# Performance work log

Measured on AMD Instinct MI355X. Metric: run time of the kernel, lower is better.

## Reference

```python
import math
import jax, jax.numpy as jnp
import numpy as np

B, T = 65536, 34
VOCAB, TOK_DIM, POS_DIM, D_MODEL, FFN_DIM, HEAD_DIM = 14, 2, 3, 5, 2, 5
EPS = 1e-5

def _pos_flat_idx():
    # replicate _build_pos_map: 10 digits, Z_HI, 10 digits, Z_HI, 10 digits, special0, special1
    sources, indices = [], []
    for _ in range(3):
        for i in range(10):
            sources.append(0); indices.append(i)
        sources.append(2); indices.append(len([s for s in sources if s == 2]) - 1)
    # fix: the torch code appends (2,0),(2,1) after first two digit blocks and (1,0),(2,2) after the third
    sources, indices = [], []
    for i in range(10): sources.append(0); indices.append(i)
    sources.append(2); indices.append(0)
    for i in range(10): sources.append(0); indices.append(i)
    sources.append(2); indices.append(1)
    for i in range(10): sources.append(0); indices.append(i)
    sources.append(1); indices.append(0)
    sources.append(2); indices.append(2)
    src = np.array(sources); idx = np.array(indices)
    # table layout: rows 0..9 digit_pos, row 10 z_hi_pos, rows 11..13 special (learned0, learned1, eos)
    offs = np.array([0, 10, 11])
    return offs[src] + idx  # (34,)

POS_FLAT = jnp.asarray(_pos_flat_idx())
CAUSAL = jnp.tril(jnp.ones((T, T), dtype=bool))

def _rms(x, w):
    return x * jax.lax.rsqrt(jnp.mean(x * x, -1, keepdims=True) + EPS) * w

def setup_inputs():
    key = jax.random.key(0)
    ks = jax.random.split(key, 16)
    n = lambda i, shape: jax.random.normal(ks[i], shape, jnp.float32) * 0.5
    return {
        'idx': jax.random.randint(ks[0], (B, T), 0, VOCAB),
        'tok_emb': n(1, (VOCAB, TOK_DIM)),
        'spiral_amp': jnp.float32(1.0),
        'spiral_phase': jnp.float32(0.1),
        'spiral_slope': jnp.float32(1.0 / 9.0),
        'spiral_offset': jnp.float32(0.05),
        'pos_corr_slope': jnp.float32(0.01),
        'pos_corr_intercept': jnp.float32(0.02),
        'z_hi_pos': n(2, (1, POS_DIM)),
        'special_pos': n(3, (2, POS_DIM)),
        'q_w': n(4, (HEAD_DIM, POS_DIM)),
        'v_w': n(5, (HEAD_DIM, TOK_DIM)),
        'out_A': n(6, (HEAD_DIM, 2)),
        'out_B': n(7, (2, D_MODEL)),
        'q_phase': n(8, (1,)),
        'ln1_w': jnp.ones((D_MODEL,), jnp.float32),
        'ln2_w': jnp.ones((D_MODEL,), jnp.float32),
        'lnf_w': jnp.ones((D_MODEL,), jnp.float32),
        'fc1_w': n(9, (FFN_DIM, D_MODEL)),
        'fc1_b': n(10, (FFN_DIM,)),
        'fc2_w': n(11, (D_MODEL, FFN_DIM)),
        'fc2_b': n(12, (D_MODEL,)),
        'head_w': n(13, (TOK_DIM, D_MODEL)),
    }

def reference(idx, tok_emb, spiral_amp, spiral_phase, spiral_slope, spiral_offset,
              pos_corr_slope, pos_corr_intercept, z_hi_pos, special_pos,
              q_w, v_w, out_A, out_B, q_phase, ln1_w, ln2_w, lnf_w,
              fc1_w, fc1_b, fc2_w, fc2_b, head_w):
    # learned spiral digit positions (10, 3)
    i = jnp.arange(10, dtype=jnp.float32)
    angle = 2.0 * math.pi * i / 10.0 + spiral_phase
    base = jnp.stack([spiral_amp * jnp.cos(angle),
                      spiral_amp * jnp.sin(angle),
                      spiral_slope * i + spiral_offset], -1)
    corr = pos_corr_intercept + pos_corr_slope * i
    digit_pos = base * (1.0 + corr)[:, None]
    table = jnp.concatenate([digit_pos, z_hi_pos, special_pos,
                             jnp.zeros((1, POS_DIM), jnp.float32)], 0)  # (14, 3)
    pos = table[POS_FLAT]  # (T, 3)

    tok = tok_emb[idx]  # (B, T, 2)
    x = jnp.concatenate([tok, jnp.broadcast_to(pos, (idx.shape[0], T, POS_DIM))], -1)  # (B,T,5)

    h = _rms(x, ln1_w)
    q = jnp.einsum('btp,dp->btd', h[..., TOK_DIM:], q_w)  # (B,T,5)
    k = q  # q_proj applied to same input for both q and k
    v = jnp.einsum('btp,dp->btd', h[..., :TOK_DIM], v_w)  # (B,T,5)

    # per-head 2D rotation on first 4 dims (HEAD_DIM//2 = 2 pairs), dim 4 unchanged
    c, s = jnp.cos(q_phase[0]), jnp.sin(q_phase[0])
    q0, q1 = q[..., 0:4:2], q[..., 1:4:2]
    q_rot = jnp.concatenate([
        jnp.stack([q0 * c - q1 * s, q0 * s + q1 * c], -1).reshape(q.shape[:-1] + (4,)),
        q[..., 4:]], -1)

    att = jnp.einsum('btd,bsd->bts', q_rot, k) / math.sqrt(HEAD_DIM)
    att = jnp.where(CAUSAL, att, -jnp.inf)
    att = jax.nn.softmax(att, -1)
    out = jnp.einsum('bts,bsd->btd', att, v)  # (B,T,5)

    x = x + (out @ out_A) @ out_B  # low-rank out_proj
    hh = _rms(x, ln2_w)
    x = x + (jax.nn.gelu(hh @ fc1_w.T + fc1_b, approximate=False) @ fc2_w.T + fc2_b)
    x = _rms(x, lnf_w)
    return (x @ head_w.T) @ tok_emb.T  # (B, T, 14)
```

## Files before the change

kernel.cpp:

```cpp
#include <hip/hip_runtime.h>
#include <math.h>

#define T_SEQ 34
#define NTOK 14
#define NE (T_SEQ * NTOK)

__global__ __launch_bounds__(256) void micro_fused_kernel(
    const int* __restrict__ idx,
    const float* __restrict__ tok_emb,
    const float* __restrict__ s_amp, const float* __restrict__ s_phase,
    const float* __restrict__ s_slope, const float* __restrict__ s_offset,
    const float* __restrict__ pc_slope, const float* __restrict__ pc_int,
    const float* __restrict__ z_hi, const float* __restrict__ spec,
    const float* __restrict__ q_w, const float* __restrict__ v_w,
    const float* __restrict__ out_A, const float* __restrict__ out_B,
    const float* __restrict__ q_phase,
    const float* __restrict__ ln1_w, const float* __restrict__ ln2_w,
    const float* __restrict__ lnf_w,
    const float* __restrict__ fc1_w, const float* __restrict__ fc1_b,
    const float* __restrict__ fc2_w, const float* __restrict__ fc2_b,
    const float* __restrict__ head_w,
    float* __restrict__ out, int N)
{
    __shared__ float H8[NE * 8];
    __shared__ float C3[NE * 4];
    __shared__ float PosT[T_SEQ * 3];
    __shared__ float TE[NTOK * 2];
    __shared__ float PMs[10];
    __shared__ float Ws[5 * NTOK];
    __shared__ float ln2s[5], lnfs[5], fc1ws[10], fc1bs[2], fc2ws[10], fc2bs[5];
    __shared__ int toks[9 * T_SEQ];

    const int tid = threadIdx.x;

    {
        const float amp = s_amp[0], ph = s_phase[0], slp = s_slope[0], off = s_offset[0];
        const float pcs = pc_slope[0], pci = pc_int[0];
        const float cph = cosf(q_phase[0]), sph = sinf(q_phase[0]);
        const float invs5 = 0.44721359549995793f;
        for (int e = tid; e < NE; e += 256) {
            int t = e / NTOK, tk = e - t * NTOK;
            float px, py, pz;
            if (t == 33)      { px = 0.f;     py = 0.f;     pz = 0.f; }
            else if (t == 32) { px = z_hi[0]; py = z_hi[1]; pz = z_hi[2]; }
            else if (t == 10) { px = spec[0]; py = spec[1]; pz = spec[2]; }
            else if (t == 21) { px = spec[3]; py = spec[4]; pz = spec[5]; }
            else {
                int i = (t < 10) ? t : (t < 21 ? t - 11 : t - 22);
                float fi = (float)i;
                float ang = 0.62831853071795864769f * fi + ph;
                float mlt = 1.f + pci + pcs * fi;
                px = amp * cosf(ang) * mlt;
                py = amp * sinf(ang) * mlt;
                pz = (slp * fi + off) * mlt;
            }
            if (tk == 0) { PosT[t*3] = px; PosT[t*3+1] = py; PosT[t*3+2] = pz; }
            float x0 = tok_emb[tk * 2], x1 = tok_emb[tk * 2 + 1];
            float ssum = x0*x0 + x1*x1 + px*px + py*py + pz*pz;
            float r = rsqrtf(ssum * 0.2f + 1e-5f);
            float h0 = x0 * r * ln1_w[0], h1 = x1 * r * ln1_w[1];
            float h2 = px * r * ln1_w[2], h3 = py * r * ln1_w[3], h4 = pz * r * ln1_w[4];
            float q0 = q_w[0]  * h2 + q_w[1]  * h3 + q_w[2]  * h4;
            float q1 = q_w[3]  * h2 + q_w[4]  * h3 + q_w[5]  * h4;
            float q2 = q_w[6]  * h2 + q_w[7]  * h3 + q_w[8]  * h4;
            float q3 = q_w[9]  * h2 + q_w[10] * h3 + q_w[11] * h4;
            float q4 = q_w[12] * h2 + q_w[13] * h3 + q_w[14] * h4;
            float r0 = q0 * cph - q1 * sph, r1 = q0 * sph + q1 * cph;
            float r2c = q2 * cph - q3 * sph, r3 = q2 * sph + q3 * cph;
            float c0 = (r0*q_w[0] + r1*q_w[3] + r2c*q_w[6] + r3*q_w[9]  + q4*q_w[12]) * invs5;
            float c1 = (r0*q_w[1] + r1*q_w[4] + r2c*q_w[7] + r3*q_w[10] + q4*q_w[13]) * invs5;
            float c2 = (r0*q_w[2] + r1*q_w[5] + r2c*q_w[8] + r3*q_w[11] + q4*q_w[14]) * invs5;
            float* H = &H8[e * 8];
            H[0] = h2; H[1] = h3; H[2] = h4; H[3] = h0; H[4] = h1;
            float* C = &C3[e * 4];
            C[0] = c0; C[1] = c1; C[2] = c2; C[3] = 0.f;
        }
    }
    if (tid < 28) TE[tid] = tok_emb[tid];
    if (tid < 70) {
        int d = tid / NTOK, v = tid - d * NTOK;
        Ws[tid] = head_w[d] * tok_emb[v * 2] + head_w[5 + d] * tok_emb[v * 2 + 1];
    }
    if (tid < 10) {
        int j = tid >> 1, c = tid & 1;
        float acc = 0.f;
        for (int i = 0; i < 5; ++i) {
            float m5 = out_A[i*2] * out_B[j] + out_A[i*2+1] * out_B[5 + j];
            acc += m5 * v_w[i*2 + c];
        }
        PMs[tid] = acc;
    }
    if (tid < 5)  { ln2s[tid] = ln2_w[tid]; lnfs[tid] = lnf_w[tid]; fc2bs[tid] = fc2_b[tid]; }
    if (tid < 10) { fc1ws[tid] = fc1_w[tid]; fc2ws[tid] = fc2_w[tid]; }
    if (tid < 2)  { fc1bs[tid] = fc1_b[tid]; }

    const int blockStart = blockIdx.x * 256;
    const int b0 = blockStart / T_SEQ;
    int lastLin = blockStart + 255; if (lastLin >= N) lastLin = N - 1;
    const int nrows = lastLin / T_SEQ - b0 + 1;
    for (int i = tid; i < nrows * T_SEQ; i += 256)
        toks[i] = idx[b0 * T_SEQ + i];

    __syncthreads();

    const int lin = blockStart + tid;
    if (lin >= N) return;
    const int b = lin / T_SEQ;
    const int t = lin - b * T_SEQ;
    const int rowBase = (b - b0) * T_SEQ;

    const int tokt = toks[rowBase + t];
    const float4 c3 = *(const float4*)&C3[(t * NTOK + tokt) * 4];
    const float xv0 = TE[tokt * 2], xv1 = TE[tokt * 2 + 1];
    const float xv2 = PosT[t*3], xv3 = PosT[t*3+1], xv4 = PosT[t*3+2];

    float l = 0.f, a0 = 0.f, a1 = 0.f;
    for (int s = 0; s <= t; ++s) {
        int o = (s * NTOK + toks[rowBase + s]) * 8;
        float4 h = *(const float4*)&H8[o];
        float h1 = H8[o + 4];
        float sc = fmaf(c3.x, h.x, fmaf(c3.y, h.y, c3.z * h.z));
        float p = __expf(sc);
        l += p;
        a0 = fmaf(p, h.w, a0);
        a1 = fmaf(p, h1, a1);
    }
    const float il = 1.f / l;
    a0 *= il; a1 *= il;

    float y[5];
#pragma unroll
    for (int j = 0; j < 5; ++j)
        y[j] = (j == 0 ? xv0 : j == 1 ? xv1 : j == 2 ? xv2 : j == 3 ? xv3 : xv4)
             + PMs[j*2] * a0 + PMs[j*2+1] * a1;

    float s2 = y[0]*y[0] + y[1]*y[1] + y[2]*y[2] + y[3]*y[3] + y[4]*y[4];
    float r2 = rsqrtf(s2 * 0.2f + 1e-5f);
    float hh[5];
#pragma unroll
    for (int j = 0; j < 5; ++j) hh[j] = y[j] * r2 * ln2s[j];

    float u0 = fc1bs[0], u1 = fc1bs[1];
#pragma unroll
    for (int j = 0; j < 5; ++j) { u0 += hh[j] * fc1ws[j]; u1 += hh[j] * fc1ws[5 + j]; }
    float g0 = 0.5f * u0 * (1.f + erff(u0 * 0.70710678118654752f));
    float g1 = 0.5f * u1 * (1.f + erff(u1 * 0.70710678118654752f));

    float y2[5]; float s3 = 0.f;
#pragma unroll
    for (int j = 0; j < 5; ++j) {
        y2[j] = y[j] + g0 * fc2ws[j * 2] + g1 * fc2ws[j * 2 + 1] + fc2bs[j];
        s3 += y2[j] * y2[j];
    }
    float r3 = rsqrtf(s3 * 0.2f + 1e-5f);
    float z[5];
#pragma unroll
    for (int j = 0; j < 5; ++j) z[j] = y2[j] * r3 * lnfs[j];

    float res[14];
#pragma unroll
    for (int v = 0; v < 14; ++v)
        res[v] = z[0] * Ws[v] + z[1] * Ws[14 + v] + z[2] * Ws[28 + v]
               + z[3] * Ws[42 + v] + z[4] * Ws[56 + v];

    float2* op = (float2*)(out + (size_t)lin * 14);
#pragma unroll
    for (int v = 0; v < 7; ++v) op[v] = make_float2(res[2 * v], res[2 * v + 1]);
}

extern "C" void kernel_launch(void* const* d_in, const int* in_sizes, int n_in,
                              void* d_out, int out_size, void* d_ws, size_t ws_size,
                              hipStream_t stream) {
    const int N = in_sizes[0];
    const int grid = (N + 255) / 256;
    micro_fused_kernel<<<grid, 256, 0, stream>>>(
        (const int*)d_in[0],
        (const float*)d_in[1], (const float*)d_in[2], (const float*)d_in[3],
        (const float*)d_in[4], (const float*)d_in[5], (const float*)d_in[6],
        (const float*)d_in[7], (const float*)d_in[8], (const float*)d_in[9],
        (const float*)d_in[10], (const float*)d_in[11], (const float*)d_in[12],
        (const float*)d_in[13], (const float*)d_in[14], (const float*)d_in[15],
        (const float*)d_in[16], (const float*)d_in[17], (const float*)d_in[18],
        (const float*)d_in[19], (const float*)d_in[20], (const float*)d_in[21],
        (const float*)d_in[22],
        (float*)d_out, N);
}
```

Baseline: 229.1 us.

## Map lanes to sequences and let each thread compute five query positions

Each block now takes 64 rows with 7 waves. Every lane owns one sequence row, and each wave handles a chunk of five query positions, so one key load is reused across five accumulators. Shared tables are split into structure-of-arrays form, tokens are stored transposed, and exp2f is used with the log2e factor folded into the precomputed query coefficients. Per-thread work is more balanced across positions than one-thread-per-token, but output stores are strided per lane (uncoalesced) and register use rises.

Result: no change. 232.1 us (+1.3%).

```diff
diff --git a/kernel.cpp b/kernel.cpp
--- a/kernel.cpp
+++ b/kernel.cpp
@@ -4,8 +4,10 @@
 #define T_SEQ 34
 #define NTOK 14
 #define NE (T_SEQ * NTOK)
-
-__global__ __launch_bounds__(256) void micro_fused_kernel(
+#define RPB 64
+#define NWAVE 7
+
+__global__ __launch_bounds__(448) void micro_fused_kernel(
     const int* __restrict__ idx,
     const float* __restrict__ tok_emb,
     const float* __restrict__ s_amp, const float* __restrict__ s_phase,
@@ -22,23 +24,27 @@
     const float* __restrict__ head_w,
     float* __restrict__ out, int N)
 {
-    __shared__ float H8[NE * 8];
-    __shared__ float C3[NE * 4];
-    __shared__ float PosT[T_SEQ * 3];
-    __shared__ float TE[NTOK * 2];
-    __shared__ float PMs[10];
-    __shared__ float Ws[5 * NTOK];
-    __shared__ float ln2s[5], lnfs[5], fc1ws[10], fc1bs[2], fc2ws[10], fc2bs[5];
-    __shared__ int toks[9 * T_SEQ];
-
-    const int tid = threadIdx.x;
+    __shared__ float2 HXY[NE];
+    __shared__ float2 HZ0[NE];
+    __shared__ float  H1s[NE];
+    __shared__ float  C3x[NE], C3y[NE], C3z[NE];
+    __shared__ float  PosX[T_SEQ], PosY[T_SEQ], PosZ[T_SEQ];
+    __shared__ float  TE[NTOK * 2];
+    __shared__ float  PMs[10];
+    __shared__ float  Ws[5 * NTOK];
+    __shared__ float  ln2s[5], lnfs[5], fc1ws[10], fc1bs[2], fc2ws[10], fc2bs[5];
+    __shared__ int    toksT[T_SEQ * RPB];
+
+    const int lane  = threadIdx.x;
+    const int chunk = threadIdx.y;
+    const int tid   = chunk * RPB + lane;
 
     {
         const float amp = s_amp[0], ph = s_phase[0], slp = s_slope[0], off = s_offset[0];
         const float pcs = pc_slope[0], pci = pc_int[0];
         const float cph = cosf(q_phase[0]), sph = sinf(q_phase[0]);
-        const float invs5 = 0.44721359549995793f;
-        for (int e = tid; e < NE; e += 256) {
+        const float escale = 0.44721359549995793f * 1.4426950408889634f;
+        for (int e = tid; e < NE; e += 448) {
             int t = e / NTOK, tk = e - t * NTOK;
             float px, py, pz;
             if (t == 33)      { px = 0.f;     py = 0.f;     pz = 0.f; }
@@ -54,7 +60,7 @@
                 py = amp * sinf(ang) * mlt;
                 pz = (slp * fi + off) * mlt;
             }
-            if (tk == 0) { PosT[t*3] = px; PosT[t*3+1] = py; PosT[t*3+2] = pz; }
+            if (tk == 0) { PosX[t] = px; PosY[t] = py; PosZ[t] = pz; }
             float x0 = tok_emb[tk * 2], x1 = tok_emb[tk * 2 + 1];
             float ssum = x0*x0 + x1*x1 + px*px + py*py + pz*pz;
             float r = rsqrtf(ssum * 0.2f + 1e-5f);
@@ -67,13 +73,12 @@
             float q4 = q_w[12] * h2 + q_w[13] * h3 + q_w[14] * h4;
             float r0 = q0 * cph - q1 * sph, r1 = q0 * sph + q1 * cph;
             float r2c = q2 * cph - q3 * sph, r3 = q2 * sph + q3 * cph;
-            float c0 = (r0*q_w[0] + r1*q_w[3] + r2c*q_w[6] + r3*q_w[9]  + q4*q_w[12]) * invs5;
-            float c1 = (r0*q_w[1] + r1*q_w[4] + r2c*q_w[7] + r3*q_w[10] + q4*q_w[13]) * invs5;
-            float c2 = (r0*q_w[2] + r1*q_w[5] + r2c*q_w[8] + r3*q_w[11] + q4*q_w[14]) * invs5;
-            float* H = &H8[e * 8];
-            H[0] = h2; H[1] = h3; H[2] = h4; H[3] = h0; H[4] = h1;
-            float* C = &C3[e * 4];
-            C[0] = c0; C[1] = c1; C[2] = c2; C[3] = 0.f;
+            C3x[e] = (r0*q_w[0] + r1*q_w[3] + r2c*q_w[6] + r3*q_w[9]  + q4*q_w[12]) * escale;
+            C3y[e] = (r0*q_w[1] + r1*q_w[4] + r2c*q_w[7] + r3*q_w[10] + q4*q_w[13]) * escale;
+            C3z[e] = (r0*q_w[2] + r1*q_w[5] + r2c*q_w[8] + r3*q_w[11] + q4*q_w[14]) * escale;
+            HXY[e] = make_float2(h2, h3);
+            HZ0[e] = make_float2(h4, h0);
+            H1s[e] = h1;
         }
     }
     if (tid < 28) TE[tid] = tok_emb[tid];
@@ -94,86 +99,120 @@
     if (tid < 10) { fc1ws[tid] = fc1_w[tid]; fc2ws[tid] = fc2_w[tid]; }
     if (tid < 2)  { fc1bs[tid] = fc1_b[tid]; }
 
-    const int blockStart = blockIdx.x * 256;
-    const int b0 = blockStart / T_SEQ;
-    int lastLin = blockStart + 255; if (lastLin >= N) lastLin = N - 1;
-    const int nrows = lastLin / T_SEQ - b0 + 1;
-    for (int i = tid; i < nrows * T_SEQ; i += 256)
-        toks[i] = idx[b0 * T_SEQ + i];
-
+    const int Brows = N / T_SEQ;
+    const int rowBase = blockIdx.x * RPB;
+    for (int j = tid; j < RPB * T_SEQ; j += 448) {
+        int r = j / T_SEQ, s = j - r * T_SEQ;
+        int rr = rowBase + r;
+        toksT[s * RPB + r] = (rr < Brows) ? idx[rr * T_SEQ + s] : 0;
+    }
     __syncthreads();
 
-    const int lin = blockStart + tid;
-    if (lin >= N) return;
-    const int b = lin / T_SEQ;
-    const int t = lin - b * T_SEQ;
-    const int rowBase = (b - b0) * T_SEQ;
-
-    const int tokt = toks[rowBase + t];
-    const float4 c3 = *(const float4*)&C3[(t * NTOK + tokt) * 4];
-    const float xv0 = TE[tokt * 2], xv1 = TE[tokt * 2 + 1];
-    const float xv2 = PosT[t*3], xv3 = PosT[t*3+1], xv4 = PosT[t*3+2];
-
-    float l = 0.f, a0 = 0.f, a1 = 0.f;
-    for (int s = 0; s <= t; ++s) {
-        int o = (s * NTOK + toks[rowBase + s]) * 8;
-        float4 h = *(const float4*)&H8[o];
-        float h1 = H8[o + 4];
-        float sc = fmaf(c3.x, h.x, fmaf(c3.y, h.y, c3.z * h.z));
-        float p = __expf(sc);
-        l += p;
-        a0 = fmaf(p, h.w, a0);
-        a1 = fmaf(p, h1, a1);
-    }
-    const float il = 1.f / l;
-    a0 *= il; a1 *= il;
-
-    float y[5];
-#pragma unroll
-    for (int j = 0; j < 5; ++j)
-        y[j] = (j == 0 ? xv0 : j == 1 ? xv1 : j == 2 ? xv2 : j == 3 ? xv3 : xv4)
-             + PMs[j*2] * a0 + PMs[j*2+1] * a1;
-
-    float s2 = y[0]*y[0] + y[1]*y[1] + y[2]*y[2] + y[3]*y[3] + y[4]*y[4];
-    float r2 = rsqrtf(s2 * 0.2f + 1e-5f);
-    float hh[5];
-#pragma unroll
-    for (int j = 0; j < 5; ++j) hh[j] = y[j] * r2 * ln2s[j];
-
-    float u0 = fc1bs[0], u1 = fc1bs[1];
-#pragma unroll
-    for (int j = 0; j < 5; ++j) { u0 += hh[j] * fc1ws[j]; u1 += hh[j] * fc1ws[5 + j]; }
-    float g0 = 0.5f * u0 * (1.f + erff(u0 * 0.70710678118654752f));
-    float g1 = 0.5f * u1 * (1.f + erff(u1 * 0.70710678118654752f));
-
-    float y2[5]; float s3 = 0.f;
+    const int t_base  = chunk * 5;
+    const int loop_end = (chunk == 6) ? 33 : (t_base + 4);
+
+    float c3x[5], c3y[5], c3z[5], L[5], A0[5], A1[5];
 #pragma unroll
     for (int j = 0; j < 5; ++j) {
-        y2[j] = y[j] + g0 * fc2ws[j * 2] + g1 * fc2ws[j * 2 + 1] + fc2bs[j];
-        s3 += y2[j] * y2[j];
-    }
-    float r3 = rsqrtf(s3 * 0.2f + 1e-5f);
-    float z[5];
-#pragma unroll
-    for (int j = 0; j < 5; ++j) z[j] = y2[j] * r3 * lnfs[j];
-
-    float res[14];
-#pragma unroll
-    for (int v = 0; v < 14; ++v)
-        res[v] = z[0] * Ws[v] + z[1] * Ws[14 + v] + z[2] * Ws[28 + v]
-               + z[3] * Ws[42 + v] + z[4] * Ws[56 + v];
-
-    float2* op = (float2*)(out + (size_t)lin * 14);
-#pragma unroll
-    for (int v = 0; v < 7; ++v) op[v] = make_float2(res[2 * v], res[2 * v + 1]);
+        L[j] = 0.f; A0[j] = 0.f; A1[j] = 0.f;
+        int t = t_base + j;
+        if (t < T_SEQ) {
+            int e = t * NTOK + toksT[t * RPB + lane];
+            c3x[j] = C3x[e]; c3y[j] = C3y[e]; c3z[j] = C3z[e];
+        } else { c3x[j] = 0.f; c3y[j] = 0.f; c3z[j] = 0.f; }
+    }
+
+    for (int s = 0; s < t_base; ++s) {
+        int e = s * NTOK + toksT[s * RPB + lane];
+        float2 hxy = HXY[e], hz0 = HZ0[e];
+        float h1 = H1s[e];
+#pragma unroll
+        for (int j = 0; j < 5; ++j) {
+            float sc = fmaf(c3x[j], hxy.x, fmaf(c3y[j], hxy.y, c3z[j] * hz0.x));
+            float p = exp2f(sc);
+            L[j] += p;
+            A0[j] = fmaf(p, hz0.y, A0[j]);
+            A1[j] = fmaf(p, h1, A1[j]);
+        }
+    }
+    for (int s = t_base; s <= loop_end; ++s) {
+        int e = s * NTOK + toksT[s * RPB + lane];
+        float2 hxy = HXY[e], hz0 = HZ0[e];
+        float h1 = H1s[e];
+#pragma unroll
+        for (int j = 0; j < 5; ++j) {
+            if (s <= t_base + j) {
+                float sc = fmaf(c3x[j], hxy.x, fmaf(c3y[j], hxy.y, c3z[j] * hz0.x));
+                float p = exp2f(sc);
+                L[j] += p;
+                A0[j] = fmaf(p, hz0.y, A0[j]);
+                A1[j] = fmaf(p, h1, A1[j]);
+            }
+        }
+    }
+
+    const int r = rowBase + lane;
+    if (r >= Brows) return;
+#pragma unroll
+    for (int j = 0; j < 5; ++j) {
+        int t = t_base + j;
+        if (t < T_SEQ) {
+            float il = 1.f / L[j];
+            float a0 = A0[j] * il, a1 = A1[j] * il;
+            int tok = toksT[t * RPB + lane];
+            float xv0 = TE[tok * 2], xv1 = TE[tok * 2 + 1];
+            float xv2 = PosX[t], xv3 = PosY[t], xv4 = PosZ[t];
+            float y[5];
+            y[0] = xv0 + PMs[0] * a0 + PMs[1] * a1;
+            y[1] = xv1 + PMs[2] * a0 + PMs[3] * a1;
+            y[2] = xv2 + PMs[4] * a0 + PMs[5] * a1;
+            y[3] = xv3 + PMs[6] * a0 + PMs[7] * a1;
+            y[4] = xv4 + PMs[8] * a0 + PMs[9] * a1;
+
+            float s2 = y[0]*y[0] + y[1]*y[1] + y[2]*y[2] + y[3]*y[3] + y[4]*y[4];
+            float r2 = rsqrtf(s2 * 0.2f + 1e-5f);
+            float hh[5];
+#pragma unroll
+            for (int k = 0; k < 5; ++k) hh[k] = y[k] * r2 * ln2s[k];
+
+            float u0 = fc1bs[0], u1 = fc1bs[1];
+#pragma unroll
+            for (int k = 0; k < 5; ++k) { u0 += hh[k] * fc1ws[k]; u1 += hh[k] * fc1ws[5 + k]; }
+            float g0 = 0.5f * u0 * (1.f + erff(u0 * 0.70710678118654752f));
+            float g1 = 0.5f * u1 * (1.f + erff(u1 * 0.70710678118654752f));
+
+            float y2[5]; float s3 = 0.f;
+#pragma unroll
+            for (int k = 0; k < 5; ++k) {
+                y2[k] = y[k] + g0 * fc2ws[k * 2] + g1 * fc2ws[k * 2 + 1] + fc2bs[k];
+                s3 += y2[k] * y2[k];
+            }
+            float r3 = rsqrtf(s3 * 0.2f + 1e-5f);
+            float z[5];
+#pragma unroll
+            for (int k = 0; k < 5; ++k) z[k] = y2[k] * r3 * lnfs[k];
+
+            float res[14];
+#pragma unroll
+            for (int v = 0; v < 14; ++v)
+                res[v] = z[0] * Ws[v] + z[1] * Ws[14 + v] + z[2] * Ws[28 + v]
+                       + z[3] * Ws[42 + v] + z[4] * Ws[56 + v];
+
+            float2* op = (float2*)(out + (size_t)(r * T_SEQ + t) * 14);
+#pragma unroll
+            for (int v = 0; v < 7; ++v) op[v] = make_float2(res[2 * v], res[2 * v + 1]);
+        }
+    }
 }
 
 extern "C" void kernel_launch(void* const* d_in, const int* in_sizes, int n_in,
                               void* d_out, int out_size, void* d_ws, size_t ws_size,
                               hipStream_t stream) {
     const int N = in_sizes[0];
-    const int grid = (N + 255) / 256;
-    micro_fused_kernel<<<grid, 256, 0, stream>>>(
+    const int Brows = N / T_SEQ;
+    dim3 block(RPB, NWAVE);
+    dim3 grid((Brows + RPB - 1) / RPB);
+    micro_fused_kernel<<<grid, block, 0, stream>>>(
         (const int*)d_in[0],
         (const float*)d_in[1], (const float*)d_in[2], (const float*)d_in[3],
         (const float*)d_in[4], (const float*)d_in[5], (const float*)d_in[6],
```
